# Optimization experiments

Measured on AMD Instinct MI355X. Metric: run time of the kernel, lower is better.

Reference implementation:

```python
import jax, jax.numpy as jnp
import numpy as np

B, V, S = 128, 64, 40
D, H, VOC = 256, 256, 20000


def setup_inputs() -> dict:
    key = jax.random.key(0)
    ks = jax.random.split(key, 26)
    g = lambda k, shp: (jax.random.normal(k, shp, dtype=jnp.float32) * 0.02)
    inp = {}
    inp['input_seqs'] = jax.random.randint(ks[0], (B, V, S), 0, VOC + 1)
    inp['mask'] = jnp.zeros((B, V), jnp.float32)
    inp['length'] = jax.random.randint(ks[1], (B,), 1, V + 1)
    inp['seq_time_step'] = jax.random.uniform(ks[2], (B, V), dtype=jnp.float32)
    inp['codemask'] = jnp.zeros((B, V, S), jnp.float32)
    inp['label'] = jax.random.randint(ks[3], (B,), 0, 2)
    # embedding table; padding_idx=-1 in torch == row VOC zeroed
    inp['emb'] = g(ks[4], (VOC + 1, D)).at[VOC].set(0.0)
    # LSTM (single layer, batch_first): torch gate order i,f,g,o
    inp['W_ih'] = g(ks[5], (4 * H, D))
    inp['W_hh'] = g(ks[6], (4 * H, H))
    inp['b_ih'] = g(ks[7], (4 * H,))
    inp['b_hh'] = g(ks[8], (4 * H,))
    # attention projections
    inp['Whk'] = g(ks[9], (D, H))
    inp['bhk'] = g(ks[10], (D,))
    inp['W1'] = g(ks[11], (64, 2 * H))
    inp['b1'] = g(ks[12], (64,))
    inp['W2'] = g(ks[13], (2, 64))
    inp['b2'] = g(ks[14], (2,))
    # classifyer MLP: d -> 4d -> 2d -> 2
    inp['C1W'] = g(ks[15], (4 * D, D))
    inp['C1b'] = g(ks[16], (4 * D,))
    inp['C2W'] = g(ks[17], (2 * D, 4 * D))
    inp['C2b'] = g(ks[18], (2 * D,))
    inp['CoW'] = g(ks[19], (2, 2 * D))
    inp['Cob'] = g(ks[20], (2,))
    return inp


def _lstm(x, W_ih, W_hh, b_ih, b_hh):
    # x: [B,T,D] -> hs: [B,T,H]; torch gate order i,f,g,o
    Bsz = x.shape[0]
    Hd = W_hh.shape[1]
    xg = jnp.einsum('btd,gd->btg', x, W_ih) + b_ih + b_hh  # [B,T,4H]

    def step(carry, xg_t):
        h, c = carry
        gates = xg_t + h @ W_hh.T
        i, f, gg, o = jnp.split(gates, 4, axis=-1)
        i = jax.nn.sigmoid(i); f = jax.nn.sigmoid(f)
        gg = jnp.tanh(gg); o = jax.nn.sigmoid(o)
        c = f * c + i * gg
        h = o * jnp.tanh(c)
        return (h, c), h

    z = jnp.zeros((Bsz, Hd), x.dtype)
    _, hs = jax.lax.scan(step, (z, z), jnp.swapaxes(xg, 0, 1))
    return jnp.swapaxes(hs, 0, 1)


def _classify(h, C1W, C1b, C2W, C2b, CoW, Cob):
    h = jax.nn.relu(h @ C1W.T + C1b)
    h = jax.nn.relu(h @ C2W.T + C2b)
    return h @ CoW.T + Cob


def reference(input_seqs, mask, length, seq_time_step, codemask, label,
              emb, W_ih, W_hh, b_ih, b_hh, Whk, bhk, W1, b1, W2, b2,
              C1W, C1b, C2W, C2b, CoW, Cob):
    # before(): embedding gather -> relu -> sum over codes (eval mode, no dropout)
    v = jax.nn.relu(emb[input_seqs]).sum(-2)  # [B,V,D]
    h = _lstm(v, W_ih, W_hh, b_ih, b_hh)       # [B,V,H]

    # vectorized form of the per-timestep attention loop:
    # bar_v[:,0]=v[:,0]; for i>=1: mix of e_k=v[:,0] and w_hk(h[:,i-1])
    e_k = v[:, :1, :]                                   # [B,1,D]
    wh = h @ Whk.T + bhk                                # [B,V,D]
    wh_prev = wh[:, :-1, :]                             # [B,V-1,D] (h at i-1)
    e_b = jnp.broadcast_to(e_k, wh_prev.shape)
    cat = jnp.concatenate([e_b, wh_prev], axis=-1)      # [B,V-1,2D]
    attn = jax.nn.softmax(jnp.tanh(cat @ W1.T + b1) @ W2.T + b2, axis=-1)
    bar_rest = e_b * attn[..., 0:1] + wh_prev * attn[..., 1:2]
    bar_v = jnp.concatenate([v[:, :1, :], bar_rest], axis=1)  # [B,V,D]

    # GAN stand-in (external injected module): identity
    Dec_V, Gen_V = bar_v, bar_v
    gen_h = _lstm(Gen_V, W_ih, W_hh, b_ih, b_hh)

    og = _classify(h, C1W, C1b, C2W, C2b, CoW, Cob)        # [B,V,2]
    fake = _classify(gen_h, C1W, C1b, C2W, C2b, CoW, Cob)  # [B,V,2]
    final_og = og[:, -1, :]
    final_fake = fake[:, -1, :]
    return (final_og, final_fake, Dec_V, Gen_V, seq_time_step, label)
```

## Files before the change

### kernel.cpp

```cpp
#include <hip/hip_runtime.h>

#define DEV __device__ __forceinline__

typedef float f32x4 __attribute__((ext_vector_type(4)));
typedef short s16x8 __attribute__((ext_vector_type(8)));
typedef short s16x4 __attribute__((ext_vector_type(4)));

DEV unsigned short f2bf(float f){
  unsigned int u = __float_as_uint(f);
  u += 0x7fffu + ((u>>16)&1u);
  return (unsigned short)(u>>16);
}
DEV float bf2f(unsigned short h){ return __uint_as_float(((unsigned int)h)<<16); }

#if __has_builtin(__builtin_amdgcn_rcpf)
DEV float frcp_(float x){ return __builtin_amdgcn_rcpf(x); }
#else
DEV float frcp_(float x){ return 1.f/x; }
#endif
#if __has_builtin(__builtin_amdgcn_exp2f)
DEV float fexp2_(float x){ return __builtin_amdgcn_exp2f(x); }
#else
DEV float fexp2_(float x){ return exp2f(x); }
#endif

DEV float tanh_(float x){
  x = fminf(x, 30.f);
  float e = fexp2_(2.8853900817779268f*x);
  return (e-1.f)*frcp_(e+1.f);
}

DEV unsigned char f2e4m3(float x){
  unsigned int u = __float_as_uint(x);
  unsigned int s = (u>>24)&0x80u;
  unsigned int mag = u & 0x7fffffffu;
  if (mag > 0x43E00000u) mag = 0x43E00000u;
  mag += 0x000FFFFFu + ((mag>>20)&1u);
  int e = (int)(mag>>23) - 120;
  unsigned int m = (mag>>20)&7u;
  unsigned int r = (e<=0) ? 0u : (((unsigned)e<<3)|m);
  return (unsigned char)(s|r);
}

DEV f32x4 mfma_bf16(s16x8 a, s16x8 b, f32x4 c){
  return __builtin_amdgcn_mfma_f32_16x16x32_bf16(a,b,c,0,0,0);
}
DEV f32x4 mfma_fp8(long a, long b, f32x4 c){
  return __builtin_amdgcn_mfma_f32_16x16x32_fp8_fp8(a,b,c,0,0,0);
}

DEV void lds_barrier(){
  asm volatile("s_waitcnt lgkmcnt(0)\n\ts_barrier" ::: "memory");
}

DEV unsigned aload_rlx(unsigned* p){
  return __hip_atomic_load(p, __ATOMIC_RELAXED, __HIP_MEMORY_SCOPE_AGENT);
}
DEV void astore_rlx(unsigned* p, unsigned v){
  __hip_atomic_store(p, v, __ATOMIC_RELAXED, __HIP_MEMORY_SCOPE_AGENT);
}
DEV void aadd_rlx(unsigned* p, unsigned v){
  __hip_atomic_fetch_add(p, v, __ATOMIC_RELAXED, __HIP_MEMORY_SCOPE_AGENT);
}
DEV void acq_fence(){ __builtin_amdgcn_fence(__ATOMIC_ACQUIRE, "agent"); }
DEV void spin_rlx(unsigned* p, unsigned tgt){
  while (aload_rlx(p) < tgt) __builtin_amdgcn_s_sleep(2);
  asm volatile("" ::: "memory");
}
DEV void block_wait(unsigned* p, unsigned tgt){
  if (threadIdx.x == 0) spin_rlx(p, tgt);
  __syncthreads();
}
DEV void block_wait_acq(unsigned* p, unsigned tgt){
  if (threadIdx.x == 0){ spin_rlx(p, tgt); acq_fence(); }
  __syncthreads();
}
DEV s16x4 aload64(const unsigned short* p){
  unsigned long long v = __hip_atomic_load((unsigned long long*)(void*)p,
      __ATOMIC_RELAXED, __HIP_MEMORY_SCOPE_AGENT);
  union { unsigned long long u; s16x4 s; } c; c.u = v; return c.s;
}
DEV void astore64(unsigned short* p, s16x4 v){
  union { s16x4 s; unsigned long long u; } c; c.s = v;
  __hip_atomic_store((unsigned long long*)(void*)p, c.u,
      __ATOMIC_RELAXED, __HIP_MEMORY_SCOPE_AGENT);
}
DEV s16x8 aload128(const unsigned short* p){
  s16x4 a = aload64(p), b = aload64(p+4);
  s16x8 r;
  r[0]=a[0]; r[1]=a[1]; r[2]=a[2]; r[3]=a[3];
  r[4]=b[0]; r[5]=b[1]; r[6]=b[2]; r[7]=b[3];
  return r;
}
DEV float aloadf(const float* p){
  return __hip_atomic_load((float*)(void*)p, __ATOMIC_RELAXED, __HIP_MEMORY_SCOPE_AGENT);
}
DEV void astoref(float* p, float v){
  __hip_atomic_store(p, v, __ATOMIC_RELAXED, __HIP_MEMORY_SCOPE_AGENT);
}
DEV void astore16(unsigned short* p, unsigned short v){
  __hip_atomic_store(p, v, __ATOMIC_RELAXED, __HIP_MEMORY_SCOPE_AGENT);
}
DEV void vm_drain(){ asm volatile("s_waitcnt vmcnt(0)" ::: "memory"); }
DEV void ntf(float* p, float v){ __builtin_nontemporal_store(v, p); }

#define Bx 128
#define Vx 64
#define Sx 40
#define Dx 256
#define Hx 256
#define NVOC 20001

#define OFF_OG   0
#define OFF_FAKE 256
#define OFF_DECV 512
#define OFF_GENV 2097664
#define OFF_STS  4194816
#define OFF_LBL  4203008

#define PW_IH  0
#define PW_HH  262144
#define PW_HK  524288
#define PW_1   589824
#define PC_1   622592
#define PC_2   884736
#define PC_O   1409024
#define P_TOT  1410048

#define HPB 264
#define BFP 272
#define WHP 272

#define FCT(t)  ((t)*32)
#define FXG(t)  (2048 + (t)*32)
#define FUC     4096
#define FXG1(t) (4352 + (t)*32)
#define XDONE   6528
#define Y1D     6656
#define Y2D     6784
#define XG1A    6912
#define FTOT    8192

__global__ void k_cvt(const float* __restrict__ emb, unsigned short* __restrict__ emb16,
                      const float* __restrict__ W_ih, const float* __restrict__ Whh,
                      const float* __restrict__ Whk, const float* __restrict__ W1,
                      const float* __restrict__ C1W, const float* __restrict__ C2W,
                      const float* __restrict__ CoW,
                      unsigned short* __restrict__ pool, unsigned char* __restrict__ whh8,
                      const float* __restrict__ sts, const int* __restrict__ label,
                      float* __restrict__ out, unsigned* __restrict__ flags){
  int bx = blockIdx.x, tid = threadIdx.x;
  if (bx < NVOC){
    size_t i = (size_t)bx*256 + tid;
    emb16[i] = f2bf(emb[i]);
    return;
  }
  if (bx < NVOC + 6532){
    int i = (bx - NVOC)*256 + tid;
    if (i < P_TOT){
      float v;
      if      (i < PW_HH) v = W_ih[i - PW_IH];
      else if (i < PW_HK) v = Whh [i - PW_HH];
      else if (i < PW_1 ) v = Whk [i - PW_HK];
      else if (i < PC_1 ) v = W1  [i - PW_1 ];
      else if (i < PC_2 ) v = C1W [i - PC_1 ];
      else if (i < PC_O ) v = C2W [i - PC_2 ];
      else                v = CoW [i - PC_O ];
      pool[i] = f2bf(v);
    } else {
      whh8[i - P_TOT] = f2e4m3(16.f*Whh[i - P_TOT]);
    }
    return;
  }
  for (int i=tid;i<FTOT;i+=256) flags[i] = 0u;
  for (int i=tid;i<Bx*Vx;i+=256) out[OFF_STS + i] = sts[i];
  if (tid < Bx) out[OFF_LBL + tid] = (float)label[tid];
}

__global__ void k_pre2(const int* __restrict__ seqs, const unsigned short* __restrict__ emb16,
                       unsigned short* __restrict__ v16,
                       float* __restrict__ decv, float* __restrict__ genv){
  int bt = blockIdx.x, d = threadIdx.x;
  const int* sp = seqs + (size_t)bt*Sx;
  float acc = 0.f;
  #pragma unroll 8
  for (int s=0;s<Sx;s++) acc += fmaxf(bf2f(emb16[(size_t)sp[s]*Dx + d]), 0.f);
  size_t o = (size_t)bt*Dx + d;
  v16[o] = f2bf(acc);
  if ((bt & 63) == 0){ decv[o] = acc; genv[o] = acc; }
}

DEV void lstm_act(const f32x4* A, float* cst, float* hv){
  const float K1 = 1.4426950408889634f/256.f;
  #pragma unroll
  for (int r=0;r<4;r++){
    float iv = frcp_(1.f + fexp2_(-K1*A[0][r]));
    float fv = frcp_(1.f + fexp2_(-K1*A[1][r]));
    float eg = fexp2_(2.f*K1*A[2][r]);
    float gv = (eg-1.f)*frcp_(eg+1.f);
    float ov = frcp_(1.f + fexp2_(-K1*A[3][r]));
    float cv = fv*cst[r] + iv*gv;
    cst[r] = cv;
    float ec = fexp2_(2.8853900817779268f*fminf(cv,30.f));
    hv[r] = ov*(ec-1.f)*frcp_(ec+1.f);
  }
}

DEV void store_h_fp8(unsigned char* hn, int q, const float* hv){
#if __has_builtin(__builtin_amdgcn_cvt_pk_fp8_f32)
  int p01 = __builtin_amdgcn_cvt_pk_fp8_f32(16.f*hv[0], 16.f*hv[1], 0, false);
  int p23 = __builtin_amdgcn_cvt_pk_fp8_f32(16.f*hv[2], 16.f*hv[3], 0, false);
  hn[(q*4+0)*HPB] = (unsigned char)p01;
  hn[(q*4+1)*HPB] = (unsigned char)(p01>>8);
  hn[(q*4+2)*HPB] = (unsigned char)p23;
  hn[(q*4+3)*HPB] = (unsigned char)(p23>>8);
#else
  #pragma unroll
  for (int r=0;r<4;r++) hn[(q*4+r)*HPB] = f2e4m3(16.f*hv[r]);
#endif
}

DEV void scan1_body(unsigned char* smem, const unsigned char* __restrict__ W8,
                    const unsigned short* __restrict__ xg1, unsigned short* __restrict__ hist,
                    int g, unsigned* __restrict__ flags){
  unsigned char*  hl  = smem;
  unsigned short* h1b = (unsigned short*)(smem + 8448);
  int tid = threadIdx.x;
  int w = tid>>6, l = tid&63, lm = l&15, q = l>>4;
  int j = w*16 + lm;
  for (int i=tid;i<8448;i+=1024) hl[i] = 0;
  long Bf[4][8];
  #pragma unroll
  for (int qq=0;qq<4;qq++){
    int n = qq*256 + j;
    #pragma unroll
    for (int kk=0;kk<8;kk++)
      Bf[qq][kk] = *(const long*)(W8 + (size_t)n*256 + kk*32 + q*8);
  }
  float cst[4] = {0.f,0.f,0.f,0.f};
  const unsigned short* xgb = xg1 + (size_t)g*16384 + q*4;
  s16x4 xc[4], xn[4];
  block_wait(&flags[FXG1(0)], 2);
  #pragma unroll
  for (int qq=0;qq<4;qq++) xc[qq] = aload64(xgb + (qq*256+j)*16);
  int all1 = 0;
  const unsigned char* hrd = hl + lm*HPB + q*8;
  #pragma unroll 1
  for (int t=0;t<Vx;t++){
    if (t > 0){
      asm volatile("s_waitcnt vmcnt(0)" ::: "memory");
      __syncthreads();
    }
    if (tid == 0){
      if (t > 0) aadd_rlx(&flags[FCT(t-1)], 1);
      if (t < Vx-1 && !all1){
        spin_rlx(&flags[FXG1(t+1)], 2);
        all1 = (aload_rlx(&flags[XG1A]) >= 128);
      }
    }
    __syncthreads();
    if (t < Vx-1){
      #pragma unroll
      for (int qq=0;qq<4;qq++)
        xn[qq] = aload64(xgb + (size_t)(t+1)*131072 + (qq*256+j)*16);
    }
    const unsigned char* hb = hrd + (t&1)*4224;
    f32x4 A[4];
    #pragma unroll
    for (int qq=0;qq<4;qq++){
      #pragma unroll
      for (int r=0;r<4;r++) A[qq][r] = bf2f((unsigned short)xc[qq][r]);
    }
    #pragma unroll
    for (int kk=0;kk<8;kk++){
      long af = *(const long*)(hb + kk*32);
      A[0] = mfma_fp8(af, Bf[0][kk], A[0]);
      A[1] = mfma_fp8(af, Bf[1][kk], A[1]);
      A[2] = mfma_fp8(af, Bf[2][kk], A[2]);
      A[3] = mfma_fp8(af, Bf[3][kk], A[3]);
    }
    float hv[4];
    lstm_act(A, cst, hv);
    store_h_fp8(hl + ((t+1)&1)*4224 + j, q, hv);
    #pragma unroll
    for (int r=0;r<4;r++) h1b[(q*4+r)*BFP + j] = f2bf(hv[r]);
    lds_barrier();
    {
      int row = tid>>6, c4 = (tid&63)*4;
      s16x4 hx = *(const s16x4*)(h1b + row*BFP + c4);
      astore64(hist + ((size_t)t*Bx + g*16 + row)*Hx + c4, hx);
    }
    #pragma unroll
    for (int qq=0;qq<4;qq++) xc[qq] = xn[qq];
  }
  asm volatile("s_waitcnt vmcnt(0)" ::: "memory");
  __syncthreads();
  if (tid == 0){ aadd_rlx(&flags[FCT(63)], 1); aadd_rlx(&flags[XDONE], 1); }
}

DEV void scan2_body(unsigned char* smem, const unsigned char* __restrict__ W8,
                    const unsigned short* __restrict__ xg2, unsigned short* __restrict__ h2,
                    int g, unsigned* __restrict__ flags){
  unsigned char*  hl  = smem;
  unsigned short* h1b = (unsigned short*)(smem + 8448);
  int tid = threadIdx.x;
  int w = tid>>6, l = tid&63, lm = l&15, q = l>>4;
  int j = w*16 + lm;
  for (int i=tid;i<8448;i+=1024) hl[i] = 0;
  long Bf[4][8];
  #pragma unroll
  for (int qq=0;qq<4;qq++){
    int n = qq*256 + j;
    #pragma unroll
    for (int kk=0;kk<8;kk++)
      Bf[qq][kk] = *(const long*)(W8 + (size_t)n*256 + kk*32 + q*8);
  }
  float cst[4] = {0.f,0.f,0.f,0.f};
  const unsigned short* xgb = xg2 + (size_t)g*16384 + q*4;
  s16x4 xc[4], xn1[4], xn2[4];
  block_wait(&flags[FXG(0)], 1);
  #pragma unroll
  for (int qq=0;qq<4;qq++) xc[qq] = aload64(xgb + (qq*256+j)*16);
  block_wait(&flags[FXG(1)], 1);
  #pragma unroll
  for (int qq=0;qq<4;qq++) xn1[qq] = aload64(xgb + 131072 + (qq*256+j)*16);
  int skip = 0;
  const unsigned char* hrd = hl + lm*HPB + q*8;
  #pragma unroll 1
  for (int t=0;t<Vx;t++){
    if (t+2 < Vx){
      if (tid == 0){
        if (!skip) spin_rlx(&flags[FXG(t+2)], 1);
        skip = (t+3 < Vx) && (aload_rlx(&flags[FXG(t+3)]) >= 1);
      }
      __syncthreads();
      #pragma unroll
      for (int qq=0;qq<4;qq++)
        xn2[qq] = aload64(xgb + (size_t)(t+2)*131072 + (qq*256+j)*16);
    }
    const unsigned char* hb = hrd + (t&1)*4224;
    f32x4 A[4];
    #pragma unroll
    for (int qq=0;qq<4;qq++){
      #pragma unroll
      for (int r=0;r<4;r++) A[qq][r] = bf2f((unsigned short)xc[qq][r]);
    }
    #pragma unroll
    for (int kk=0;kk<8;kk++){
      long af = *(const long*)(hb + kk*32);
      A[0] = mfma_fp8(af, Bf[0][kk], A[0]);
      A[1] = mfma_fp8(af, Bf[1][kk], A[1]);
      A[2] = mfma_fp8(af, Bf[2][kk], A[2]);
      A[3] = mfma_fp8(af, Bf[3][kk], A[3]);
    }
    float hv[4];
    lstm_act(A, cst, hv);
    store_h_fp8(hl + ((t+1)&1)*4224 + j, q, hv);
    if (t == Vx-1){
      #pragma unroll
      for (int r=0;r<4;r++) h1b[(q*4+r)*BFP + j] = f2bf(hv[r]);
      lds_barrier();
      {
        int row = tid>>6, c4 = (tid&63)*4;
        s16x4 hx = *(const s16x4*)(h1b + row*BFP + c4);
        astore64(h2 + (size_t)(g*16 + row)*Hx + c4, hx);
      }
      asm volatile("s_waitcnt vmcnt(0)" ::: "memory");
      __syncthreads();
      if (tid == 0) aadd_rlx(&flags[XDONE], 1);
    } else {
      lds_barrier();
    }
    #pragma unroll
    for (int qq=0;qq<4;qq++){ xc[qq] = xn1[qq]; xn1[qq] = xn2[qq]; }
  }
}

template<int ALDS>
DEV void xg2_tile(const unsigned short* Ab, const unsigned short* __restrict__ pool,
                  const float* __restrict__ b_ih, const float* __restrict__ b_hh,
                  unsigned short* __restrict__ xg2, int tile, int w, int lm, int q){
  int mh = (w&1)*64, nb = (w>>1)*128;
  #pragma unroll 1
  for (int sc=0; sc<4; sc++){
    int n0 = nb + sc*32;
    f32x4 acc[4][2];
    #pragma unroll
    for (int nt=0;nt<2;nt++){
      int n = n0 + nt*16 + lm;
      float bz = b_ih[n] + b_hh[n];
      #pragma unroll
      for (int mt=0;mt<4;mt++) acc[mt][nt] = (f32x4){bz,bz,bz,bz};
    }
    #pragma unroll
    for (int kk=0;kk<8;kk++){
      s16x8 bfr[2];
      #pragma unroll
      for (int nt=0;nt<2;nt++){
        int n = n0 + nt*16 + lm;
        bfr[nt] = *(const s16x8*)(pool + PW_IH + (size_t)n*256 + kk*32 + q*8);
      }
      #pragma unroll
      for (int mt=0;mt<4;mt++){
        int row = mh + mt*16 + lm;
        s16x8 afr = ALDS ? *(const s16x8*)(Ab + (size_t)row*WHP + kk*32 + q*8)
                         : *(const s16x8*)(Ab + (size_t)row*Vx*Dx + kk*32 + q*8);
        acc[mt][0] = mfma_bf16(afr, bfr[0], acc[mt][0]);
        acc[mt][1] = mfma_bf16(afr, bfr[1], acc[mt][1]);
      }
    }
    #pragma unroll
    for (int mt=0;mt<4;mt++){
      int m = mh + mt*16 + q*4;
      int gg = m>>4;
      #pragma unroll
      for (int nt=0;nt<2;nt++){
        int n = n0 + nt*16 + lm;
        s16x4 sv;
        #pragma unroll
        for (int r=0;r<4;r++) sv[r] = (short)f2bf(256.f*acc[mt][nt][r]);
        astore64(xg2 + (((size_t)tile*8 + gg)*1024 + n)*16 + (m&15), sv);
      }
    }
  }
}

DEV void worker_body(unsigned short* whs, int t,
    const unsigned short* __restrict__ hist1, const unsigned short* __restrict__ v16,
    const float* __restrict__ u, const unsigned short* __restrict__ pool,
    const float* __restrict__ bhk, const float* __restrict__ W2, const float* __restrict__ b2,
    const float* __restrict__ b_ih, const float* __restrict__ b_hh,
    float* __restrict__ decv, float* __restrict__ genv,
    unsigned short* __restrict__ xg2, unsigned* __restrict__ flags){
  int tid = threadIdx.x, w = tid>>6, l = tid&63, lm = l&15, q = l>>4;
  if (t == 63){
    xg2_tile<0>(v16, pool, b_ih, b_hh, xg2, 0, w, lm, q);
    vm_drain();
    __syncthreads();
    if (tid == 0) astore_rlx(&flags[FXG(0)], 1);
    return;
  }
  block_wait(&flags[FCT(t)], 8);
  {
    int r0 = (w&7)*16, n0 = (w>>3)*128;
    const unsigned short* Ar = hist1 + ((size_t)t*Bx + r0 + lm)*Hx;
    f32x4 acc[8];
    #pragma unroll
    for (int nt=0;nt<8;nt++){
      float bz = bhk[n0 + nt*16 + lm];
      acc[nt] = (f32x4){bz,bz,bz,bz};
    }
    #pragma unroll
    for (int kk=0;kk<8;kk++){
      s16x8 afr = aload128(Ar + kk*32 + q*8);
      #pragma unroll
      for (int nt=0;nt<8;nt++){
        int n = n0 + nt*16 + lm;
        s16x8 bfr = *(const s16x8*)(pool + PW_HK + (size_t)n*256 + kk*32 + q*8);
        acc[nt] = mfma_bf16(afr, bfr, acc[nt]);
      }
    }
    #pragma unroll
    for (int nt=0;nt<8;nt++){
      int n = n0 + nt*16 + lm, mb = r0 + q*4;
      #pragma unroll
      for (int r=0;r<4;r++) whs[(size_t)(mb+r)*WHP + n] = f2bf(acc[nt][r]);
    }
  }
  if (tid == 0) spin_rlx(&flags[FUC], 8);
  __syncthreads();
  if (w < 8){
    int m0l = w*16;
    f32x4 a2[4];
    #pragma unroll
    for (int nt=0;nt<4;nt++){
      int n = nt*16 + lm;
      #pragma unroll
      for (int r=0;r<4;r++) a2[nt][r] = aloadf(u + (size_t)(m0l + q*4 + r)*64 + n);
    }
    #pragma unroll
    for (int kk=0;kk<8;kk++){
      s16x8 afr = *(const s16x8*)(whs + (size_t)(m0l+lm)*WHP + kk*32 + q*8);
      #pragma unroll
      for (int nt=0;nt<4;nt++){
        int n = nt*16 + lm;
        s16x8 bfr = *(const s16x8*)(pool + PW_1 + (size_t)n*512 + 256 + kk*32 + q*8);
        a2[nt] = mfma_bf16(afr, bfr, a2[nt]);
      }
    }
    float p0a[4] = {0,0,0,0}, p1a[4] = {0,0,0,0};
    #pragma unroll
    for (int nt=0;nt<4;nt++){
      int n = nt*16 + lm;
      float w2a = W2[n], w2b = W2[64+n];
      #pragma unroll
      for (int r=0;r<4;r++){
        float z = tanh_(a2[nt][r]);
        p0a[r] += z*w2a; p1a[r] += z*w2b;
      }
    }
    #pragma unroll
    for (int s=1;s<16;s<<=1){
      #pragma unroll
      for (int r=0;r<4;r++){ p0a[r] += __shfl_xor(p0a[r], s, 16); p1a[r] += __shfl_xor(p1a[r], s, 16); }
    }
    float bb0 = b2[0], bb1 = b2[1];
    int d0 = lm*16;
    #pragma unroll
    for (int r=0;r<4;r++){
      int b = m0l + q*4 + r;
      float g0 = p0a[r]+bb0, g1 = p1a[r]+bb1;
      float al0 = frcp_(1.f + fexp2_(1.4426950408889634f*(g1-g0)));
      float al1 = 1.f - al0;
      const unsigned short* ek = v16 + (size_t)b*Vx*Dx + d0;
      unsigned short* whp = whs + (size_t)b*WHP + d0;
      size_t ob = ((size_t)b*Vx + (t+1))*Dx + d0;
      #pragma unroll
      for (int c=0;c<2;c++){
        s16x8 e8 = *(const s16x8*)(ek + c*8);
        s16x8 w8 = *(const s16x8*)(whp + c*8);
        s16x8 o16;
        #pragma unroll
        for (int jj=0;jj<8;jj++){
          float o = al0*bf2f((unsigned short)e8[jj]) + al1*bf2f((unsigned short)w8[jj]);
          ntf(decv + ob + c*8 + jj, o);
          ntf(genv + ob + c*8 + jj, o);
          o16[jj] = (short)f2bf(o);
        }
        *(s16x8*)(whp + c*8) = o16;
      }
    }
  }
  __syncthreads();
  xg2_tile<1>(whs, pool, b_ih, b_hh, xg2, t+1, w, lm, q);
  vm_drain();
  __syncthreads();
  if (tid == 0) astore_rlx(&flags[FXG(t+1)], 1);
}

DEV void xg1_body(const unsigned short* __restrict__ v16, const unsigned short* __restrict__ pool,
                  const float* __restrict__ b_ih, const float* __restrict__ b_hh,
                  unsigned short* __restrict__ xg1, int blk, unsigned* __restrict__ flags){
  int tid = threadIdx.x, w = tid>>6, l = tid&63, lm = l&15, q = l>>4;
  int m0 = blk*64;
  int n0 = w*64;
  f32x4 acc[4][4];
  #pragma unroll
  for (int nt=0;nt<4;nt++){
    int n = n0 + nt*16 + lm;
    float bz = b_ih[n] + b_hh[n];
    #pragma unroll
    for (int mt=0;mt<4;mt++) acc[mt][nt] = (f32x4){bz,bz,bz,bz};
  }
  const s16x8* Arow[4];
  #pragma unroll
  for (int mt=0;mt<4;mt++){
    int m = m0 + mt*16 + lm;
    Arow[mt] = (const s16x8*)(v16 + ((size_t)(m&127)*Vx + (m>>7))*(size_t)Dx);
  }
  for (int kk=0; kk<8; kk++){
    s16x8 bfr[4];
    #pragma unroll
    for (int nt=0;nt<4;nt++){
      int n = n0 + nt*16 + lm;
      bfr[nt] = *(const s16x8*)(pool + PW_IH + (size_t)n*256 + kk*32 + q*8);
    }
    #pragma unroll
    for (int mt=0;mt<4;mt++){
      s16x8 afr = Arow[mt][kk*4 + q];
      #pragma unroll
      for (int nt=0;nt<4;nt++)
        acc[mt][nt] = mfma_bf16(afr, bfr[nt], acc[mt][nt]);
    }
  }
  #pragma unroll
  for (int mt=0;mt<4;mt++){
    int mbase = m0 + mt*16 + q*4;
    int tt = mbase>>7, bb = mbase&127;
    int gg = bb>>4;
    #pragma unroll
    for (int nt=0;nt<4;nt++){
      int n = n0 + nt*16 + lm;
      s16x4 sv;
      #pragma unroll
      for (int r=0;r<4;r++) sv[r] = (short)f2bf(256.f*acc[mt][nt][r]);
      astore64(xg1 + (((size_t)tt*8 + gg)*1024 + n)*16 + (bb&15), sv);
    }
  }
  vm_drain();
  __syncthreads();
  if (tid == 0){ aadd_rlx(&flags[FXG1(blk>>1)], 1); aadd_rlx(&flags[XG1A], 1); }
}

DEV void cls_gemm(const unsigned short* __restrict__ A, const unsigned short* __restrict__ Bw,
                  const float* __restrict__ bias, unsigned short* __restrict__ C,
                  int K, int Ntot, int bxx, int byy){
  int tid = threadIdx.x, w = tid>>6, l = tid&63, lm = l&15, q = l>>4;
  int m0 = bxx*64, n0 = byy*256 + w*64;
  f32x4 acc[4][4];
  #pragma unroll
  for (int nt=0;nt<4;nt++){
    int n = n0 + nt*16 + lm;
    float bz = bias[n];
    #pragma unroll
    for (int mt=0;mt<4;mt++) acc[mt][nt] = (f32x4){bz,bz,bz,bz};
  }
  const s16x8* Arow[4];
  #pragma unroll
  for (int mt=0;mt<4;mt++)
    Arow[mt] = (const s16x8*)(A + (size_t)(m0 + mt*16 + lm)*K);
  int kkn = K/32;
  for (int kk=0; kk<kkn; kk++){
    s16x8 bfr[4];
    #pragma unroll
    for (int nt=0;nt<4;nt++){
      int n = n0 + nt*16 + lm;
      bfr[nt] = *(const s16x8*)(Bw + (size_t)n*K + kk*32 + q*8);
    }
    #pragma unroll
    for (int mt=0;mt<4;mt++){
      s16x8 afr = Arow[mt][kk*4 + q];
      #pragma unroll
      for (int nt=0;nt<4;nt++)
        acc[mt][nt] = mfma_bf16(afr, bfr[nt], acc[mt][nt]);
    }
  }
  #pragma unroll
  for (int mt=0;mt<4;mt++){
    int mbase = m0 + mt*16 + q*4;
    #pragma unroll
    for (int nt=0;nt<4;nt++){
      int n = n0 + nt*16 + lm;
      #pragma unroll
      for (int r=0;r<4;r++)
        astore16(C + (size_t)(mbase+r)*Ntot + n, f2bf(fmaxf(acc[mt][nt][r], 0.f)));
    }
  }
}

__global__ __launch_bounds__(1024) void k_mega(
    const unsigned char* __restrict__ W8,
    unsigned short* __restrict__ xg1, unsigned short* __restrict__ xg2,
    unsigned short* __restrict__ hist1,
    const unsigned short* __restrict__ v16, float* __restrict__ u,
    const unsigned short* __restrict__ pool,
    const float* __restrict__ bhk, const float* __restrict__ W2, const float* __restrict__ b2,
    const float* __restrict__ b1, const float* __restrict__ b_ih, const float* __restrict__ b_hh,
    const float* __restrict__ C1b, const float* __restrict__ C2b, const float* __restrict__ Cob,
    float* __restrict__ decv, float* __restrict__ genv, float* __restrict__ out,
    unsigned* __restrict__ flags){
  __shared__ __align__(16) unsigned char smem[69632];
  int blk = blockIdx.x;
  unsigned short* X  = hist1 + (size_t)(Vx-1)*Bx*Hx;
  unsigned short* h2 = hist1 + (size_t)Vx*Bx*Hx;
  unsigned short* y1 = xg1;
  unsigned short* y2 = xg1 + 262144;
  if (blk < 8){
    scan1_body(smem, W8, xg1, hist1, blk, flags);
  } else if (blk < 16){
    scan2_body(smem, W8, xg2, h2, blk-8, flags);
  } else if (blk < 80){
    worker_body((unsigned short*)smem, blk-16, hist1, v16, u, pool, bhk, W2, b2,
                b_ih, b_hh, decv, genv, xg2, flags);
  } else if (blk < 88){
    int t2 = (blk-80)*1024 + threadIdx.x;
    int b = t2>>6, n = t2&63;
    const s16x8* vr = (const s16x8*)(v16 + (size_t)b*Vx*Dx);
    const s16x8* wr = (const s16x8*)(pool + PW_1 + (size_t)n*512);
    float a = b1[n];
    for (int kk=0;kk<32;kk++){
      s16x8 x = vr[kk], ww = wr[kk];
      #pragma unroll
      for (int jj=0;jj<8;jj++) a += bf2f((unsigned short)x[jj])*bf2f((unsigned short)ww[jj]);
    }
    astoref(u + t2, a);
    vm_drain();
    __syncthreads();
    if (threadIdx.x == 0) aadd_rlx(&flags[FUC], 1);
  } else if (blk < 216){
    xg1_body(v16, pool, b_ih, b_hh, xg1, blk-88, flags);
  } else if (blk < 232){
    block_wait_acq(&flags[XDONE], 16);
    int p = blk-216;
    if (threadIdx.x < 256) cls_gemm(X, pool+PC_1, C1b, y1, 256, 1024, p&3, p>>2);
    vm_drain();
    __syncthreads();
    if (threadIdx.x == 0) aadd_rlx(&flags[Y1D], 1);
  } else if (blk < 240){
    block_wait_acq(&flags[Y1D], 16);
    int p = blk-232;
    if (threadIdx.x < 256) cls_gemm(y1, pool+PC_2, C2b, y2, 1024, 512, p&3, p>>2);
    vm_drain();
    __syncthreads();
    if (threadIdx.x == 0) aadd_rlx(&flags[Y2D], 1);
  } else {
    block_wait_acq(&flags[Y2D], 8);
    if (threadIdx.x < 256){
      int t2 = (blk-240)*256 + threadIdx.x;
      int m = t2>>1, n = t2&1;
      const s16x8* yr = (const s16x8*)(y2 + (size_t)m*512);
      const s16x8* wr = (const s16x8*)(pool + PC_O + (size_t)n*512);
      float a = Cob[n];
      for (int kk=0;kk<64;kk++){
        s16x8 yv = yr[kk], ww = wr[kk];
        #pragma unroll
        for (int jj=0;jj<8;jj++) a += bf2f((unsigned short)yv[jj])*bf2f((unsigned short)ww[jj]);
      }
      int base = (m < 128) ? (OFF_OG + m*2) : (OFF_FAKE + (m-128)*2);
      out[base + n] = a;
    }
  }
}

extern "C" void kernel_launch(void* const* d_in, const int* in_sizes, int n_in,
                              void* d_out, int out_size, void* d_ws, size_t ws_size,
                              hipStream_t stream) {
  const int*   seqs  = (const int*)d_in[0];
  const float* sts   = (const float*)d_in[3];
  const int*   label = (const int*)d_in[5];
  const float* emb   = (const float*)d_in[6];
  const float* W_ih  = (const float*)d_in[7];
  const float* W_hh  = (const float*)d_in[8];
  const float* b_ih  = (const float*)d_in[9];
  const float* b_hh  = (const float*)d_in[10];
  const float* Whk   = (const float*)d_in[11];
  const float* bhk   = (const float*)d_in[12];
  const float* W1    = (const float*)d_in[13];
  const float* b1    = (const float*)d_in[14];
  const float* W2    = (const float*)d_in[15];
  const float* b2    = (const float*)d_in[16];
  const float* C1b   = (const float*)d_in[18];
  const float* C2b   = (const float*)d_in[20];
  const float* Cob   = (const float*)d_in[22];
  float* out = (float*)d_out;

  char* ws = (char*)d_ws;
  unsigned short* v16    = (unsigned short*)(ws + 0);
  unsigned short* xg1    = (unsigned short*)(ws + (4<<20));
  unsigned short* hist1  = (unsigned short*)(ws + (20<<20));
  unsigned short* xg2    = (unsigned short*)(ws + (25<<20));
  unsigned short* emb16  = xg2;
  float*          u      = (float*)(ws + (41<<20));
  unsigned char*  whh8   = (unsigned char*)(ws + (41<<20) + (64<<10));
  unsigned*       flags  = (unsigned*)(ws + (41<<20) + (384<<10));
  unsigned short* pool   = (unsigned short*)(ws + (42<<20));

  float* decv = out + OFF_DECV;
  float* genv = out + OFF_GENV;

  k_cvt<<<dim3(NVOC + 6532 + 1), dim3(256), 0, stream>>>(emb, emb16,
      W_ih, W_hh, Whk, W1, (const float*)d_in[17], (const float*)d_in[19],
      (const float*)d_in[21], pool, whh8, sts, label, out, flags);
  k_pre2<<<dim3(8192), dim3(256), 0, stream>>>(seqs, emb16, v16, decv, genv);
  k_mega<<<dim3(242), dim3(1024), 0, stream>>>(whh8, xg1, xg2, hist1, v16, u, pool,
      bhk, W2, b2, b1, b_ih, b_hh, C1b, C2b, Cob, decv, genv, out, flags);
}
```

Measured before the change: 508.9 us.

## Fuse embedding conversion and gather into persistent megakernel front stage

Removes the standalone embedding-to-bf16 pass from k_cvt and the k_pre2 gather kernel. The 128 xg1 blocks of the megakernel now convert the embedding table cooperatively, sync on a counter, gather and sum embeddings for one timestep into LDS, and feed that straight into the input-projection GEMM. This cuts a kernel launch and the v16 global round trip for most timesteps. It also turns xg2 into an 8-slot ring buffer guarded by a new scan2 progress flag, and swaps some atomic loads for plain loads. The trade-off is more inter-block spin-waiting and tighter coupling between producers and consumers.

```diff
diff --git a/kernel.cpp b/kernel.cpp
--- a/kernel.cpp
+++ b/kernel.cpp
@@ -85,16 +85,6 @@
   __hip_atomic_store((unsigned long long*)(void*)p, c.u,
       __ATOMIC_RELAXED, __HIP_MEMORY_SCOPE_AGENT);
 }
-DEV s16x8 aload128(const unsigned short* p){
-  s16x4 a = aload64(p), b = aload64(p+4);
-  s16x8 r;
-  r[0]=a[0]; r[1]=a[1]; r[2]=a[2]; r[3]=a[3];
-  r[4]=b[0]; r[5]=b[1]; r[6]=b[2]; r[7]=b[3];
-  return r;
-}
-DEV float aloadf(const float* p){
-  return __hip_atomic_load((float*)(void*)p, __ATOMIC_RELAXED, __HIP_MEMORY_SCOPE_AGENT);
-}
 DEV void astoref(float* p, float v){
   __hip_atomic_store(p, v, __ATOMIC_RELAXED, __HIP_MEMORY_SCOPE_AGENT);
 }
@@ -130,6 +120,7 @@
 #define HPB 264
 #define BFP 272
 #define WHP 272
+#define VTP 264
 
 #define FCT(t)  ((t)*32)
 #define FXG(t)  (2048 + (t)*32)
@@ -139,10 +130,12 @@
 #define Y1D     6656
 #define Y2D     6784
 #define XG1A    6912
+#define EMBC    7040
+#define FEK     7168
+#define SC2P    7296
 #define FTOT    8192
 
-__global__ void k_cvt(const float* __restrict__ emb, unsigned short* __restrict__ emb16,
-                      const float* __restrict__ W_ih, const float* __restrict__ Whh,
+__global__ void k_cvt(const float* __restrict__ W_ih, const float* __restrict__ Whh,
                       const float* __restrict__ Whk, const float* __restrict__ W1,
                       const float* __restrict__ C1W, const float* __restrict__ C2W,
                       const float* __restrict__ CoW,
@@ -150,13 +143,8 @@
                       const float* __restrict__ sts, const int* __restrict__ label,
                       float* __restrict__ out, unsigned* __restrict__ flags){
   int bx = blockIdx.x, tid = threadIdx.x;
-  if (bx < NVOC){
-    size_t i = (size_t)bx*256 + tid;
-    emb16[i] = f2bf(emb[i]);
-    return;
-  }
-  if (bx < NVOC + 6532){
-    int i = (bx - NVOC)*256 + tid;
+  if (bx < 6532){
+    int i = bx*256 + tid;
     if (i < P_TOT){
       float v;
       if      (i < PW_HH) v = W_ih[i - PW_IH];
@@ -177,19 +165,6 @@
   if (tid < Bx) out[OFF_LBL + tid] = (float)label[tid];
 }
 
-__global__ void k_pre2(const int* __restrict__ seqs, const unsigned short* __restrict__ emb16,
-                       unsigned short* __restrict__ v16,
-                       float* __restrict__ decv, float* __restrict__ genv){
-  int bt = blockIdx.x, d = threadIdx.x;
-  const int* sp = seqs + (size_t)bt*Sx;
-  float acc = 0.f;
-  #pragma unroll 8
-  for (int s=0;s<Sx;s++) acc += fmaxf(bf2f(emb16[(size_t)sp[s]*Dx + d]), 0.f);
-  size_t o = (size_t)bt*Dx + d;
-  v16[o] = f2bf(acc);
-  if ((bt & 63) == 0){ decv[o] = acc; genv[o] = acc; }
-}
-
 DEV void lstm_act(const f32x4* A, float* cst, float* hv){
   const float K1 = 1.4426950408889634f/256.f;
   #pragma unroll
@@ -242,7 +217,7 @@
   s16x4 xc[4], xn[4];
   block_wait(&flags[FXG1(0)], 2);
   #pragma unroll
-  for (int qq=0;qq<4;qq++) xc[qq] = aload64(xgb + (qq*256+j)*16);
+  for (int qq=0;qq<4;qq++) xc[qq] = *(const s16x4*)(xgb + (qq*256+j)*16);
   int all1 = 0;
   const unsigned char* hrd = hl + lm*HPB + q*8;
   #pragma unroll 1
@@ -262,7 +237,7 @@
     if (t < Vx-1){
       #pragma unroll
       for (int qq=0;qq<4;qq++)
-        xn[qq] = aload64(xgb + (size_t)(t+1)*131072 + (qq*256+j)*16);
+        xn[qq] = *(const s16x4*)(xgb + (size_t)(t+1)*131072 + (qq*256+j)*16);
     }
     const unsigned char* hb = hrd + (t&1)*4224;
     f32x4 A[4];
@@ -316,14 +291,16 @@
       Bf[qq][kk] = *(const long*)(W8 + (size_t)n*256 + kk*32 + q*8);
   }
   float cst[4] = {0.f,0.f,0.f,0.f};
-  const unsigned short* xgb = xg2 + (size_t)g*16384 + q*4;
+  const unsigned short* xgb = xg2 + q*4;
   s16x4 xc[4], xn1[4], xn2[4];
   block_wait(&flags[FXG(0)], 1);
   #pragma unroll
-  for (int qq=0;qq<4;qq++) xc[qq] = aload64(xgb + (qq*256+j)*16);
+  for (int qq=0;qq<4;qq++)
+    xc[qq] = aload64(xgb + (size_t)g*16384 + (qq*256+j)*16);
   block_wait(&flags[FXG(1)], 1);
   #pragma unroll
-  for (int qq=0;qq<4;qq++) xn1[qq] = aload64(xgb + 131072 + (qq*256+j)*16);
+  for (int qq=0;qq<4;qq++)
+    xn1[qq] = aload64(xgb + 131072 + (size_t)g*16384 + (qq*256+j)*16);
   int skip = 0;
   const unsigned char* hrd = hl + lm*HPB + q*8;
   #pragma unroll 1
@@ -336,7 +313,7 @@
       __syncthreads();
       #pragma unroll
       for (int qq=0;qq<4;qq++)
-        xn2[qq] = aload64(xgb + (size_t)(t+2)*131072 + (qq*256+j)*16);
+        xn2[qq] = aload64(xgb + (size_t)((t+2)&7)*131072 + (size_t)g*16384 + (qq*256+j)*16);
     }
     const unsigned char* hb = hrd + (t&1)*4224;
     f32x4 A[4];
@@ -371,6 +348,7 @@
     } else {
       lds_barrier();
     }
+    if (tid == 0) aadd_rlx(&flags[SC2P], 1);
     #pragma unroll
     for (int qq=0;qq<4;qq++){ xc[qq] = xn1[qq]; xn1[qq] = xn2[qq]; }
   }
@@ -419,7 +397,7 @@
         s16x4 sv;
         #pragma unroll
         for (int r=0;r<4;r++) sv[r] = (short)f2bf(256.f*acc[mt][nt][r]);
-        astore64(xg2 + (((size_t)tile*8 + gg)*1024 + n)*16 + (m&15), sv);
+        astore64(xg2 + (((size_t)(tile&7)*8 + gg)*1024 + n)*16 + (m&15), sv);
       }
     }
   }
@@ -434,6 +412,7 @@
     unsigned short* __restrict__ xg2, unsigned* __restrict__ flags){
   int tid = threadIdx.x, w = tid>>6, l = tid&63, lm = l&15, q = l>>4;
   if (t == 63){
+    block_wait(&flags[FEK], 2);
     xg2_tile<0>(v16, pool, b_ih, b_hh, xg2, 0, w, lm, q);
     vm_drain();
     __syncthreads();
@@ -452,7 +431,7 @@
     }
     #pragma unroll
     for (int kk=0;kk<8;kk++){
-      s16x8 afr = aload128(Ar + kk*32 + q*8);
+      s16x8 afr = *(const s16x8*)(Ar + kk*32 + q*8);
       #pragma unroll
       for (int nt=0;nt<8;nt++){
         int n = n0 + nt*16 + lm;
@@ -476,7 +455,7 @@
     for (int nt=0;nt<4;nt++){
       int n = nt*16 + lm;
       #pragma unroll
-      for (int r=0;r<4;r++) a2[nt][r] = aloadf(u + (size_t)(m0l + q*4 + r)*64 + n);
+      for (int r=0;r<4;r++) a2[nt][r] = u[(size_t)(m0l + q*4 + r)*64 + n];
     }
     #pragma unroll
     for (int kk=0;kk<8;kk++){
@@ -532,17 +511,77 @@
     }
   }
   __syncthreads();
+  if (t+1 >= 8) block_wait(&flags[SC2P], (unsigned)(8*(t+1-7)));
   xg2_tile<1>(whs, pool, b_ih, b_hh, xg2, t+1, w, lm, q);
   vm_drain();
   __syncthreads();
   if (tid == 0) astore_rlx(&flags[FXG(t+1)], 1);
 }
 
-DEV void xg1_body(const unsigned short* __restrict__ v16, const unsigned short* __restrict__ pool,
-                  const float* __restrict__ b_ih, const float* __restrict__ b_hh,
-                  unsigned short* __restrict__ xg1, int blk, unsigned* __restrict__ flags){
-  int tid = threadIdx.x, w = tid>>6, l = tid&63, lm = l&15, q = l>>4;
-  int m0 = blk*64;
+DEV void front_body(unsigned short* vt, int f,
+    const float* __restrict__ emb, unsigned short* __restrict__ emb16,
+    const int* __restrict__ seqs, unsigned short* __restrict__ v16,
+    const unsigned short* __restrict__ pool,
+    const float* __restrict__ b_ih, const float* __restrict__ b_hh,
+    float* __restrict__ decv, float* __restrict__ genv,
+    unsigned short* __restrict__ xg1, unsigned* __restrict__ flags){
+  int tid = threadIdx.x;
+  {
+    int u0 = f*10001, u1 = u0+10001;
+    if (u1 > 1280064) u1 = 1280064;
+    for (int uu = u0 + tid; uu < u1; uu += 1024){
+      const float* src = emb + (size_t)uu*4;
+      s16x4 pk;
+      #pragma unroll
+      for (int i=0;i<4;i++) pk[i] = (short)f2bf(src[i]);
+      astore64(emb16 + (size_t)uu*4, pk);
+    }
+    vm_drain();
+    __syncthreads();
+    if (tid == 0) aadd_rlx(&flags[EMBC], 1);
+  }
+  block_wait(&flags[EMBC], 128);
+  int t = f>>1, bh = (f&1)*64;
+  int sub = tid>>8, d = tid&255;
+  #pragma unroll 1
+  for (int ib=0; ib<4; ib++){
+    int rl0 = ib*16 + sub;
+    const int* sp0 = seqs + ((size_t)(bh+rl0   )*Vx + t)*Sx;
+    const int* sp1 = seqs + ((size_t)(bh+rl0+ 4)*Vx + t)*Sx;
+    const int* sp2 = seqs + ((size_t)(bh+rl0+ 8)*Vx + t)*Sx;
+    const int* sp3 = seqs + ((size_t)(bh+rl0+12)*Vx + t)*Sx;
+    float a0=0.f, a1=0.f, a2=0.f, a3=0.f;
+    #pragma unroll 8
+    for (int s=0;s<Sx;s++){
+      a0 += fmaxf(bf2f(emb16[(size_t)sp0[s]*Dx + d]), 0.f);
+      a1 += fmaxf(bf2f(emb16[(size_t)sp1[s]*Dx + d]), 0.f);
+      a2 += fmaxf(bf2f(emb16[(size_t)sp2[s]*Dx + d]), 0.f);
+      a3 += fmaxf(bf2f(emb16[(size_t)sp3[s]*Dx + d]), 0.f);
+    }
+    vt[(rl0   )*VTP + d] = f2bf(a0);
+    vt[(rl0+ 4)*VTP + d] = f2bf(a1);
+    vt[(rl0+ 8)*VTP + d] = f2bf(a2);
+    vt[(rl0+12)*VTP + d] = f2bf(a3);
+    if (t == 0){
+      ntf(decv + (size_t)(bh+rl0   )*Vx*Dx + d, a0);
+      ntf(genv + (size_t)(bh+rl0   )*Vx*Dx + d, a0);
+      ntf(decv + (size_t)(bh+rl0+ 4)*Vx*Dx + d, a1);
+      ntf(genv + (size_t)(bh+rl0+ 4)*Vx*Dx + d, a1);
+      ntf(decv + (size_t)(bh+rl0+ 8)*Vx*Dx + d, a2);
+      ntf(genv + (size_t)(bh+rl0+ 8)*Vx*Dx + d, a2);
+      ntf(decv + (size_t)(bh+rl0+12)*Vx*Dx + d, a3);
+      ntf(genv + (size_t)(bh+rl0+12)*Vx*Dx + d, a3);
+    }
+  }
+  lds_barrier();
+  if (t == 0){
+    for (int uu = tid; uu < 4096; uu += 1024){
+      int rl = uu>>6, c4 = (uu&63)*4;
+      s16x4 ev = *(const s16x4*)(vt + rl*VTP + c4);
+      astore64(v16 + (size_t)(bh+rl)*Vx*Dx + c4, ev);
+    }
+  }
+  int w = tid>>6, l = tid&63, lm = l&15, q = l>>4;
   int n0 = w*64;
   f32x4 acc[4][4];
   #pragma unroll
@@ -552,12 +591,6 @@
     #pragma unroll
     for (int mt=0;mt<4;mt++) acc[mt][nt] = (f32x4){bz,bz,bz,bz};
   }
-  const s16x8* Arow[4];
-  #pragma unroll
-  for (int mt=0;mt<4;mt++){
-    int m = m0 + mt*16 + lm;
-    Arow[mt] = (const s16x8*)(v16 + ((size_t)(m&127)*Vx + (m>>7))*(size_t)Dx);
-  }
   for (int kk=0; kk<8; kk++){
     s16x8 bfr[4];
     #pragma unroll
@@ -567,7 +600,7 @@
     }
     #pragma unroll
     for (int mt=0;mt<4;mt++){
-      s16x8 afr = Arow[mt][kk*4 + q];
+      s16x8 afr = *(const s16x8*)(vt + (size_t)(mt*16+lm)*VTP + kk*32 + q*8);
       #pragma unroll
       for (int nt=0;nt<4;nt++)
         acc[mt][nt] = mfma_bf16(afr, bfr[nt], acc[mt][nt]);
@@ -575,7 +608,7 @@
   }
   #pragma unroll
   for (int mt=0;mt<4;mt++){
-    int mbase = m0 + mt*16 + q*4;
+    int mbase = f*64 + mt*16 + q*4;
     int tt = mbase>>7, bb = mbase&127;
     int gg = bb>>4;
     #pragma unroll
@@ -589,7 +622,11 @@
   }
   vm_drain();
   __syncthreads();
-  if (tid == 0){ aadd_rlx(&flags[FXG1(blk>>1)], 1); aadd_rlx(&flags[XG1A], 1); }
+  if (tid == 0){
+    aadd_rlx(&flags[FXG1(t)], 1);
+    aadd_rlx(&flags[XG1A], 1);
+    if (t == 0) aadd_rlx(&flags[FEK], 1);
+  }
 }
 
 DEV void cls_gemm(const unsigned short* __restrict__ A, const unsigned short* __restrict__ Bw,
@@ -642,8 +679,10 @@
     const unsigned char* __restrict__ W8,
     unsigned short* __restrict__ xg1, unsigned short* __restrict__ xg2,
     unsigned short* __restrict__ hist1,
-    const unsigned short* __restrict__ v16, float* __restrict__ u,
+    unsigned short* __restrict__ v16, float* __restrict__ u,
     const unsigned short* __restrict__ pool,
+    const float* __restrict__ emb, unsigned short* __restrict__ emb16,
+    const int* __restrict__ seqs,
     const float* __restrict__ bhk, const float* __restrict__ W2, const float* __restrict__ b2,
     const float* __restrict__ b1, const float* __restrict__ b_ih, const float* __restrict__ b_hh,
     const float* __restrict__ C1b, const float* __restrict__ C2b, const float* __restrict__ Cob,
@@ -663,6 +702,7 @@
     worker_body((unsigned short*)smem, blk-16, hist1, v16, u, pool, bhk, W2, b2,
                 b_ih, b_hh, decv, genv, xg2, flags);
   } else if (blk < 88){
+    block_wait(&flags[FEK], 2);
     int t2 = (blk-80)*1024 + threadIdx.x;
     int b = t2>>6, n = t2&63;
     const s16x8* vr = (const s16x8*)(v16 + (size_t)b*Vx*Dx);
@@ -678,7 +718,8 @@
     __syncthreads();
     if (threadIdx.x == 0) aadd_rlx(&flags[FUC], 1);
   } else if (blk < 216){
-    xg1_body(v16, pool, b_ih, b_hh, xg1, blk-88, flags);
+    front_body((unsigned short*)smem, blk-88, emb, emb16, seqs, v16, pool,
+               b_ih, b_hh, decv, genv, xg1, flags);
   } else if (blk < 232){
     block_wait_acq(&flags[XDONE], 16);
     int p = blk-216;
@@ -739,19 +780,19 @@
   unsigned short* xg1    = (unsigned short*)(ws + (4<<20));
   unsigned short* hist1  = (unsigned short*)(ws + (20<<20));
   unsigned short* xg2    = (unsigned short*)(ws + (25<<20));
-  unsigned short* emb16  = xg2;
-  float*          u      = (float*)(ws + (41<<20));
-  unsigned char*  whh8   = (unsigned char*)(ws + (41<<20) + (64<<10));
-  unsigned*       flags  = (unsigned*)(ws + (41<<20) + (384<<10));
-  unsigned short* pool   = (unsigned short*)(ws + (42<<20));
+  unsigned short* emb16  = (unsigned short*)(ws + (27<<20));
+  float*          u      = (float*)(ws + (37<<20));
+  unsigned char*  whh8   = (unsigned char*)(ws + (37<<20) + (64<<10));
+  unsigned*       flags  = (unsigned*)(ws + (37<<20) + (384<<10));
+  unsigned short* pool   = (unsigned short*)(ws + (38<<20));
 
   float* decv = out + OFF_DECV;
   float* genv = out + OFF_GENV;
 
-  k_cvt<<<dim3(NVOC + 6532 + 1), dim3(256), 0, stream>>>(emb, emb16,
-      W_ih, W_hh, Whk, W1, (const float*)d_in[17], (const float*)d_in[19],
-      (const float*)d_in[21], pool, whh8, sts, label, out, flags);
-  k_pre2<<<dim3(8192), dim3(256), 0, stream>>>(seqs, emb16, v16, decv, genv);
+  k_cvt<<<dim3(6533), dim3(256), 0, stream>>>(W_ih, W_hh, Whk, W1,
+      (const float*)d_in[17], (const float*)d_in[19], (const float*)d_in[21],
+      pool, whh8, sts, label, out, flags);
   k_mega<<<dim3(242), dim3(1024), 0, stream>>>(whh8, xg1, xg2, hist1, v16, u, pool,
-      bhk, W2, b2, b1, b_ih, b_hh, C1b, C2b, Cob, decv, genv, out, flags);
-}
+      emb, emb16, seqs, bhk, W2, b2, b1, b_ih, b_hh, C1b, C2b, Cob,
+      decv, genv, out, flags);
+}
```

New measurement: 707.2 us. +39.0%, slower.
